# Optimization experiments

Hardware: AMD Instinct MI355X
Metric: run time of the kernel (lower is better)

Reference implementation:

```python
import jax, jax.numpy as jnp
import numpy as np

N = 25000      # nodes
E = 400000     # directed edges (avg degree 16)
FN = 32        # node feature dim
FE = 16        # edge feature dim
H = 16         # hidden_state_size
M = 16         # message_size
ITERS = 3      # mp_iterations


def setup_inputs() -> dict:
    key = jax.random.key(0)
    ks = jax.random.split(key, 16)
    s = 0.1
    return {
        "node_features": jax.random.normal(ks[0], (N, FN), jnp.float32),
        "edge_features": jax.random.normal(ks[1], (E, FE), jnp.float32),
        # Initial dense
        "W_init": jax.random.normal(ks[2], (FN, H), jnp.float32) * s,
        "b_init": jnp.zeros((H,), jnp.float32),
        # edge_net dense: FE -> M*H
        "W_edge": jax.random.normal(ks[3], (FE, M * H), jnp.float32) * s,
        "b_edge": jnp.zeros((M * H,), jnp.float32),
        # GRU (keras default, reset_after=True), input dim 1, units H, gate order z|r|h
        "Wi_gru": jax.random.normal(ks[4], (1, 3 * H), jnp.float32) * s,
        "Wh_gru": jax.random.normal(ks[5], (H, 3 * H), jnp.float32) * s,
        "bi_gru": jnp.zeros((3 * H,), jnp.float32),
        "bh_gru": jnp.zeros((3 * H,), jnp.float32),
        # Readout denses -> 1 output
        "W_ri": jax.random.normal(ks[6], (2 * H, 1), jnp.float32) * s,
        "b_ri": jnp.zeros((1,), jnp.float32),
        "W_rj": jax.random.normal(ks[7], (H, 1), jnp.float32) * s,
        "b_rj": jnp.zeros((1,), jnp.float32),
        # graph structure (directed edges): message to `receivers[e]` from `senders[e]`
        "receivers": jax.random.randint(ks[8], (E,), 0, N, jnp.int32),
        "senders": jax.random.randint(ks[9], (E,), 0, N, jnp.int32),
    }


def _gru_seq(seq, Wi, Wh, bi, bh):
    # seq: [N, T] sequence of scalars per node; keras GRU, reset_after=True, units=H
    n = seq.shape[0]
    xs = seq.T[:, :, None]  # [T, N, 1]
    h0 = jnp.zeros((n, H), seq.dtype)

    def step(h, x_t):
        gx = x_t @ Wi + bi            # [N, 3H]
        gh = h @ Wh + bh              # [N, 3H]
        xz, xr, xh = jnp.split(gx, 3, axis=1)
        hz, hr, hh = jnp.split(gh, 3, axis=1)
        z = jax.nn.sigmoid(xz + hz)
        r = jax.nn.sigmoid(xr + hr)
        hcand = jnp.tanh(xh + r * hh)
        h_new = z * h + (1.0 - z) * hcand
        return h_new, None

    h_final, _ = jax.lax.scan(step, h0, xs)
    return h_final


def reference(node_features, edge_features, W_init, b_init, W_edge, b_edge,
              Wi_gru, Wh_gru, bi_gru, bh_gru, W_ri, b_ri, W_rj, b_rj,
              receivers, senders):
    # Initial hidden state
    hidden0 = node_features @ W_init + b_init   # [N, H]
    hidden = hidden0

    # edge_net(edge) reshaped to per-edge matrices [E, M, H] (constant across iterations)
    edge_mats = (edge_features @ W_edge + b_edge).reshape(E, M, H)

    for _ in range(ITERS):
        h_nb = hidden[senders]                                  # [E, H]
        msg = jnp.einsum("emh,eh->em", edge_mats, h_nb)        # [E, M] matvec per edge
        messages = jax.ops.segment_sum(msg, receivers, num_segments=N)  # sum aggregation
        seq = jnp.concatenate([hidden, messages], axis=1)       # [N, H+M]
        hidden = _gru_seq(seq, Wi_gru, Wh_gru, bi_gru, bh_gru)  # [N, H]

    # Readout
    i = jnp.concatenate([hidden, hidden0], axis=1) @ W_ri + b_ri  # [N, 1]
    j = hidden @ W_rj + b_rj                                      # [N, 1]
    return jnp.sum(i * j, axis=0)                                 # [1]
```

## Files before the change

kernel.cpp:

```cpp
#include <hip/hip_runtime.h>

#define N_NODES 25000
#define N_EDGES 400000

__device__ __forceinline__ float fast_sigmoid(float x) {
    return __builtin_amdgcn_rcpf(1.0f + __expf(-x));
}
__device__ __forceinline__ float fast_tanh(float x) {
    return 1.0f - 2.0f * __builtin_amdgcn_rcpf(__expf(2.0f * x) + 1.0f);
}

#define SWZF(x, k) __int_as_float(__builtin_amdgcn_ds_swizzle(__float_as_int(x), ((k) << 10) | 0x1F))
#define BCAST16(x, t) __int_as_float(__builtin_amdgcn_ds_swizzle(__float_as_int(x), ((t) << 5) | 0x10))

__global__ void __launch_bounds__(256) k_init(
        const float* __restrict__ nf, const float* __restrict__ Wini,
        const float* __restrict__ bini,
        float* __restrict__ hidden0, float* __restrict__ hid,
        int* __restrict__ cnt, int* __restrict__ rcnt)
{
    int gtid = blockIdx.x * 256 + threadIdx.x;
    if (gtid <= N_NODES) { cnt[gtid] = 0; rcnt[gtid] = 0; }
    int node = gtid >> 4;
    int j = gtid & 15;
    if (node >= N_NODES) return;

    const float4* nf4 = (const float4*)(nf + node * 32);
    float acc = bini[j];
#pragma unroll
    for (int g = 0; g < 8; ++g) {
        float4 v = nf4[g];
        acc = fmaf(v.x, Wini[(g*4+0)*16 + j], acc);
        acc = fmaf(v.y, Wini[(g*4+1)*16 + j], acc);
        acc = fmaf(v.z, Wini[(g*4+2)*16 + j], acc);
        acc = fmaf(v.w, Wini[(g*4+3)*16 + j], acc);
    }
    hidden0[node*16 + j] = acc;
    hid[node*16 + j] = acc;
}

__global__ void __launch_bounds__(256) k_rank(const int* __restrict__ send,
        const int* __restrict__ recv,
        int* __restrict__ cnt, int* __restrict__ rcnt,
        int* __restrict__ rank_s, int* __restrict__ rank_r)
{
    int e = blockIdx.x * 256 + threadIdx.x;
    if (e < N_EDGES) {
        rank_s[e] = atomicAdd(&cnt[send[e]], 1);
        rank_r[e] = atomicAdd(&rcnt[recv[e]], 1);
    }
}

#define SCAN_TOT 25600
__global__ void __launch_bounds__(1024) k_scan2(
        const int* __restrict__ cnt,  int* __restrict__ row_ptr,
        const int* __restrict__ rcnt, int* __restrict__ rrow_ptr,
        float* __restrict__ out)
{
    __shared__ int data[SCAN_TOT];
    __shared__ int sums[1024];
    int t = threadIdx.x;
    const int CH = 25;

    const int* SRC = blockIdx.x ? rcnt : cnt;
    int* DST = blockIdx.x ? rrow_ptr : row_ptr;

    for (int i = t; i < SCAN_TOT; i += 1024)
        data[i] = (i < N_NODES) ? SRC[i] : 0;
    __syncthreads();

    int base = t * CH;
    int s = 0;
#pragma unroll
    for (int i = 0; i < CH; ++i) s += data[base + i];
    sums[t] = s;
    __syncthreads();

    for (int off = 1; off < 1024; off <<= 1) {
        int add = (t >= off) ? sums[t - off] : 0;
        __syncthreads();
        sums[t] += add;
        __syncthreads();
    }
    int run = sums[t] - s;

#pragma unroll
    for (int i = 0; i < CH; ++i) {
        int v = data[base + i];
        data[base + i] = run;
        run += v;
    }
    __syncthreads();

    for (int i = t; i < N_NODES; i += 1024)
        DST[i] = data[i];
    if (t == 0) {
        if (blockIdx.x == 0) { row_ptr[N_NODES] = N_EDGES; out[0] = 0.0f; }
        else                 { rrow_ptr[N_NODES] = N_EDGES; }
    }
}

__global__ void __launch_bounds__(256) k_place(const int* __restrict__ send,
        const int* __restrict__ recv,
        const int* __restrict__ rank_s, const int* __restrict__ rank_r,
        const int* __restrict__ row_ptr, const int* __restrict__ rrow_ptr,
        int* __restrict__ ipos, int* __restrict__ rp)
{
    int e = blockIdx.x * 256 + threadIdx.x;
    if (e < N_EDGES) {
        int pos = row_ptr[send[e]] + rank_s[e];
        ipos[e] = pos;
        rp[pos] = rrow_ptr[recv[e]] + rank_r[e];
    }
}

__global__ void __launch_bounds__(256) k_permute(const float* __restrict__ ef,
        const int* __restrict__ ipos, float* __restrict__ efp)
{
    int gtid = blockIdx.x * 256 + threadIdx.x;
    int e = gtid >> 4;
    int c = gtid & 15;
    if (e < N_EDGES) efp[(size_t)ipos[e]*16 + c] = ef[(size_t)e*16 + c];
}

#define MCHUNK 512
#define MSG16(E0,E1,E2,E3) ( \
    ( fmaf((E0).w,q[3],  fmaf((E0).z,q[2],  fmaf((E0).y,q[1],  fmaf((E0).x,q[0],  qb)))) \
    + fmaf((E1).w,q[7],  fmaf((E1).z,q[6],  fmaf((E1).y,q[5],  fmaf((E1).x,q[4],  0.0f)))) ) \
  + ( fmaf((E2).w,q[11], fmaf((E2).z,q[10], fmaf((E2).y,q[9],  fmaf((E2).x,q[8],  0.0f)))) \
    + fmaf((E3).w,q[15], fmaf((E3).z,q[14], fmaf((E3).y,q[13], fmaf((E3).x,q[12], 0.0f)))) ) )

__global__ void __launch_bounds__(256) k_msg(
        const float* __restrict__ hid, const float* __restrict__ efp,
        const int* __restrict__ rp,
        const float* __restrict__ We, const float* __restrict__ be,
        const int* __restrict__ row_ptr,
        float* __restrict__ tmp)
{
    __shared__ float sef[MCHUNK * 16];
    __shared__ int   srp[MCHUNK];
    int tid = threadIdx.x;
    int grp = tid >> 4;
    int m   = tid & 15;
    int s   = blockIdx.x * 16 + grp;
    bool active = (s < N_NODES);
    int sc = active ? s : 0;

    int s0 = blockIdx.x * 16;
    int blk_beg = row_ptr[s0];
    int s1 = s0 + 16; if (s1 > N_NODES) s1 = N_NODES;
    int blk_end = row_ptr[s1];

    int beg = active ? row_ptr[s]     : 0;
    int end = active ? row_ptr[s + 1] : 0;

    float h[16];
    {
        const float4* h4 = (const float4*)(hid + sc*16);
        float4 a = h4[0], b = h4[1], c = h4[2], d = h4[3];
        h[0]=a.x; h[1]=a.y; h[2]=a.z;  h[3]=a.w;
        h[4]=b.x; h[5]=b.y; h[6]=b.z;  h[7]=b.w;
        h[8]=c.x; h[9]=c.y; h[10]=c.z; h[11]=c.w;
        h[12]=d.x; h[13]=d.y; h[14]=d.z; h[15]=d.w;
    }
    float q[16];
#pragma unroll
    for (int f = 0; f < 16; ++f) {
        const float4* wf = (const float4*)(We + f*256 + m*16);
        float4 a = wf[0], b = wf[1], c = wf[2], d = wf[3];
        float acc;
        acc  = a.x*h[0]  + a.y*h[1]  + a.z*h[2]  + a.w*h[3];
        acc += b.x*h[4]  + b.y*h[5]  + b.z*h[6]  + b.w*h[7];
        acc += c.x*h[8]  + c.y*h[9]  + c.z*h[10] + c.w*h[11];
        acc += d.x*h[12] + d.y*h[13] + d.z*h[14] + d.w*h[15];
        q[f] = acc;
    }
    float qb;
    {
        const float4* bf = (const float4*)(be + m*16);
        float4 a = bf[0], b = bf[1], c = bf[2], d = bf[3];
        qb  = a.x*h[0]  + a.y*h[1]  + a.z*h[2]  + a.w*h[3];
        qb += b.x*h[4]  + b.y*h[5]  + b.z*h[6]  + b.w*h[7];
        qb += c.x*h[8]  + c.y*h[9]  + c.z*h[10] + c.w*h[11];
        qb += d.x*h[12] + d.y*h[13] + d.z*h[14] + d.w*h[15];
    }

    for (int cbeg = blk_beg; cbeg < blk_end; cbeg += MCHUNK) {
        int cend = cbeg + MCHUNK; if (cend > blk_end) cend = blk_end;
        int nedge = cend - cbeg;
        int nfl = nedge * 4;
        __syncthreads();
        {
            const float4* gsrc = (const float4*)(efp + (size_t)cbeg * 16);
            float4* ldst = (float4*)sef;
            for (int i = tid; i < nfl; i += 256) ldst[i] = gsrc[i];
            for (int i = tid; i < nedge; i += 256) srp[i] = rp[cbeg + i];
        }
        __syncthreads();

        int lo = beg > cbeg ? beg : cbeg;
        int hi = end < cend ? end : cend;
        int i = lo;
        for (; i + 2 <= hi; i += 2) {
            const float4* l0 = (const float4*)(sef + (size_t)(i   - cbeg) * 16);
            const float4* l1 = (const float4*)(sef + (size_t)(i+1 - cbeg) * 16);
            float4 A0=l0[0], A1=l0[1], A2=l0[2], A3=l0[3];
            float4 B0=l1[0], B1=l1[1], B2=l1[2], B3=l1[3];
            int r0 = srp[i   - cbeg];
            int r1 = srp[i+1 - cbeg];
            float v0 = MSG16(A0, A1, A2, A3);
            float v1 = MSG16(B0, B1, B2, B3);
            tmp[(size_t)r0*16 + m] = v0;
            tmp[(size_t)r1*16 + m] = v1;
        }
        for (; i < hi; ++i) {
            const float4* l0 = (const float4*)(sef + (size_t)(i - cbeg) * 16);
            float4 A0=l0[0], A1=l0[1], A2=l0[2], A3=l0[3];
            int r0 = srp[i - cbeg];
            tmp[(size_t)r0*16 + m] = MSG16(A0, A1, A2, A3);
        }
    }
}

__global__ void __launch_bounds__(256) k_gru(
        const float* __restrict__ hid_in, const float* __restrict__ tmp,
        const int* __restrict__ rrow_ptr,
        const float* __restrict__ Wi, const float* __restrict__ Wh,
        const float* __restrict__ bi, const float* __restrict__ bh,
        float* __restrict__ hid_out)
{
    int gtid = blockIdx.x * 256 + threadIdx.x;
    int node = gtid >> 4;
    int j = gtid & 15;
    if (node >= N_NODES) return;

    float s0 = 0.0f, s1 = 0.0f, s2 = 0.0f, s3 = 0.0f;
    {
        int beg = rrow_ptr[node];
        int end = rrow_ptr[node + 1];
        const float* p = tmp + (size_t)beg * 16 + j;
        int d = end - beg;
        int i = 0;
        for (; i + 8 <= d; i += 8) {
            float a0 = p[(i+0)*16];
            float a1 = p[(i+1)*16];
            float a2 = p[(i+2)*16];
            float a3 = p[(i+3)*16];
            float a4 = p[(i+4)*16];
            float a5 = p[(i+5)*16];
            float a6 = p[(i+6)*16];
            float a7 = p[(i+7)*16];
            s0 += a0; s1 += a1; s2 += a2; s3 += a3;
            s0 += a4; s1 += a5; s2 += a6; s3 += a7;
        }
        for (; i < d; ++i) s0 += p[i*16];
    }
    float msg_own = (s0 + s1) + (s2 + s3);
    float h_own = hid_in[node*16 + j];

    float Wz[16], Wr[16], Wc[16];
#pragma unroll
    for (int k = 0; k < 16; ++k) {
        int l = j ^ k;
        Wz[k] = Wh[l*48 + j];
        Wr[k] = Wh[l*48 + 16 + j];
        Wc[k] = Wh[l*48 + 32 + j];
    }
    float Wiz = Wi[j], Wir = Wi[16+j], Wih = Wi[32+j];
    float cz   = bi[j] + bh[j];
    float cr   = bi[16+j] + bh[16+j];
    float bih_ = bi[32+j];
    float bhh_ = bh[32+j];

    float hn = 0.0f;

#define STEPK(k) { float v = SWZF(hn, k); \
        az = fmaf(v, Wz[k], az); ar = fmaf(v, Wr[k], ar); ac = fmaf(v, Wc[k], ac); }

#define GRUSTEP(XV) { \
        float xv = (XV); \
        float az = fmaf(xv, Wiz, cz); \
        float ar = fmaf(xv, Wir, cr); \
        float ac = bhh_; \
        az = fmaf(hn, Wz[0], az); \
        ar = fmaf(hn, Wr[0], ar); \
        ac = fmaf(hn, Wc[0], ac); \
        STEPK(1)  STEPK(2)  STEPK(3)  STEPK(4)  STEPK(5) \
        STEPK(6)  STEPK(7)  STEPK(8)  STEPK(9)  STEPK(10) \
        STEPK(11) STEPK(12) STEPK(13) STEPK(14) STEPK(15) \
        float z  = fast_sigmoid(az); \
        float r  = fast_sigmoid(ar); \
        float hc = fast_tanh(fmaf(xv, Wih, bih_) + r * ac); \
        hn = fmaf(z, hn - hc, hc); }

    GRUSTEP(BCAST16(h_own, 0))  GRUSTEP(BCAST16(h_own, 1))
    GRUSTEP(BCAST16(h_own, 2))  GRUSTEP(BCAST16(h_own, 3))
    GRUSTEP(BCAST16(h_own, 4))  GRUSTEP(BCAST16(h_own, 5))
    GRUSTEP(BCAST16(h_own, 6))  GRUSTEP(BCAST16(h_own, 7))
    GRUSTEP(BCAST16(h_own, 8))  GRUSTEP(BCAST16(h_own, 9))
    GRUSTEP(BCAST16(h_own, 10)) GRUSTEP(BCAST16(h_own, 11))
    GRUSTEP(BCAST16(h_own, 12)) GRUSTEP(BCAST16(h_own, 13))
    GRUSTEP(BCAST16(h_own, 14)) GRUSTEP(BCAST16(h_own, 15))
    GRUSTEP(BCAST16(msg_own, 0))  GRUSTEP(BCAST16(msg_own, 1))
    GRUSTEP(BCAST16(msg_own, 2))  GRUSTEP(BCAST16(msg_own, 3))
    GRUSTEP(BCAST16(msg_own, 4))  GRUSTEP(BCAST16(msg_own, 5))
    GRUSTEP(BCAST16(msg_own, 6))  GRUSTEP(BCAST16(msg_own, 7))
    GRUSTEP(BCAST16(msg_own, 8))  GRUSTEP(BCAST16(msg_own, 9))
    GRUSTEP(BCAST16(msg_own, 10)) GRUSTEP(BCAST16(msg_own, 11))
    GRUSTEP(BCAST16(msg_own, 12)) GRUSTEP(BCAST16(msg_own, 13))
    GRUSTEP(BCAST16(msg_own, 14)) GRUSTEP(BCAST16(msg_own, 15))
#undef GRUSTEP
#undef STEPK

    hid_out[node*16 + j] = hn;
}

__global__ void __launch_bounds__(256) k_readout(
        const float* __restrict__ hid, const float* __restrict__ hid0,
        const float* __restrict__ Wri, const float* __restrict__ bri,
        const float* __restrict__ Wrj, const float* __restrict__ brj,
        float* __restrict__ out)
{
    int n = blockIdx.x * 256 + threadIdx.x;
    float val = 0.0f;
    if (n < N_NODES) {
        const float4* h4 = (const float4*)(hid + n * 16);
        const float4* g4 = (const float4*)(hid0 + n * 16);
        float iv = bri[0];
        float jv = brj[0];
#pragma unroll
        for (int g = 0; g < 4; ++g) {
            float4 h  = h4[g];
            float4 h0 = g4[g];
            iv = fmaf(h.x,  Wri[g*4+0], iv);  iv = fmaf(h.y,  Wri[g*4+1], iv);
            iv = fmaf(h.z,  Wri[g*4+2], iv);  iv = fmaf(h.w,  Wri[g*4+3], iv);
            iv = fmaf(h0.x, Wri[16+g*4+0], iv); iv = fmaf(h0.y, Wri[16+g*4+1], iv);
            iv = fmaf(h0.z, Wri[16+g*4+2], iv); iv = fmaf(h0.w, Wri[16+g*4+3], iv);
            jv = fmaf(h.x,  Wrj[g*4+0], jv);  jv = fmaf(h.y,  Wrj[g*4+1], jv);
            jv = fmaf(h.z,  Wrj[g*4+2], jv);  jv = fmaf(h.w,  Wrj[g*4+3], jv);
        }
        val = iv * jv;
    }
#pragma unroll
    for (int off = 32; off > 0; off >>= 1)
        val += __shfl_xor(val, off, 64);
    __shared__ float wsum[4];
    int w = threadIdx.x >> 6;
    if ((threadIdx.x & 63) == 0) wsum[w] = val;
    __syncthreads();
    if (threadIdx.x == 0)
        atomicAdd(out, wsum[0] + wsum[1] + wsum[2] + wsum[3]);
}

extern "C" void kernel_launch(void* const* d_in, const int* in_sizes, int n_in,
                              void* d_out, int out_size, void* d_ws, size_t ws_size,
                              hipStream_t stream)
{
    const float* node_features = (const float*)d_in[0];
    const float* edge_features = (const float*)d_in[1];
    const float* W_init = (const float*)d_in[2];
    const float* b_init = (const float*)d_in[3];
    const float* W_edge = (const float*)d_in[4];
    const float* b_edge = (const float*)d_in[5];
    const float* Wi_gru = (const float*)d_in[6];
    const float* Wh_gru = (const float*)d_in[7];
    const float* bi_gru = (const float*)d_in[8];
    const float* bh_gru = (const float*)d_in[9];
    const float* W_ri = (const float*)d_in[10];
    const float* b_ri = (const float*)d_in[11];
    const float* W_rj = (const float*)d_in[12];
    const float* b_rj = (const float*)d_in[13];
    const int* receivers = (const int*)d_in[14];
    const int* senders   = (const int*)d_in[15];
    float* out = (float*)d_out;

    float* fb      = (float*)d_ws;
    float* hidden0 = fb;
    float* hidA    = fb + 400000;
    float* hidB    = fb + 800000;
    float* tmp     = fb + 1200000;
    float* efp     = fb + 7600000;
    int* ib       = (int*)(fb + 14000000);
    int* cnt      = ib;
    int* row_ptr  = ib + 25024;
    int* rcnt     = ib + 50048;
    int* rrow_ptr = ib + 75072;
    int* ipos     = ib + 100096;
    int* rp       = ib + 500096;
    int* rank_s   = ib + 900096;
    int* rank_r   = ib + 1300096;

    dim3 b256(256);
    int grid_n16 = (N_NODES * 16 + 255) / 256;
    int grid_e   = (N_EDGES + 255) / 256;
    int grid_e16 = (N_EDGES * 16 + 255) / 256;
    int grid_n   = (N_NODES + 255) / 256;
    int grid_blk = (N_NODES + 15) / 16;

    k_init<<<grid_n16, b256, 0, stream>>>(node_features, W_init, b_init,
                                          hidden0, hidA, cnt, rcnt);
    k_rank<<<grid_e, b256, 0, stream>>>(senders, receivers, cnt, rcnt,
                                        rank_s, rank_r);
    k_scan2<<<2, 1024, 0, stream>>>(cnt, row_ptr, rcnt, rrow_ptr, out);
    k_place<<<grid_e, b256, 0, stream>>>(senders, receivers, rank_s, rank_r,
                                         row_ptr, rrow_ptr, ipos, rp);
    k_permute<<<grid_e16, b256, 0, stream>>>(edge_features, ipos, efp);

    float* hin = hidA;
    float* hout = hidB;
    for (int it = 0; it < 3; ++it) {
        k_msg<<<grid_blk, b256, 0, stream>>>(hin, efp, rp,
                                             W_edge, b_edge, row_ptr, tmp);
        k_gru<<<grid_n16, b256, 0, stream>>>(hin, tmp, rrow_ptr,
                                             Wi_gru, Wh_gru, bi_gru, bh_gru, hout);
        float* t = hin; hin = hout; hout = t;
    }

    k_readout<<<grid_n, b256, 0, stream>>>(hin, hidden0, W_ri, b_ri, W_rj, b_rj, out);
}
```

Baseline: 405.3 us.

## Process two nodes per GRU thread and fuse edge permute into placement

```diff
diff --git a/kernel.cpp b/kernel.cpp
--- a/kernel.cpp
+++ b/kernel.cpp
@@ -2,6 +2,7 @@
 
 #define N_NODES 25000
 #define N_EDGES 400000
+#define NHALF   12500
 
 __device__ __forceinline__ float fast_sigmoid(float x) {
     return __builtin_amdgcn_rcpf(1.0f + __expf(-x));
@@ -11,7 +12,7 @@
 }
 
 #define SWZF(x, k) __int_as_float(__builtin_amdgcn_ds_swizzle(__float_as_int(x), ((k) << 10) | 0x1F))
-#define BCAST16(x, t) __int_as_float(__builtin_amdgcn_ds_swizzle(__float_as_int(x), ((t) << 5) | 0x10))
+#define BPERM(x, a) __int_as_float(__builtin_amdgcn_ds_bpermute((a), __float_as_int(x)))
 
 __global__ void __launch_bounds__(256) k_init(
         const float* __restrict__ nf, const float* __restrict__ Wini,
@@ -104,23 +105,18 @@
         const int* __restrict__ recv,
         const int* __restrict__ rank_s, const int* __restrict__ rank_r,
         const int* __restrict__ row_ptr, const int* __restrict__ rrow_ptr,
-        int* __restrict__ ipos, int* __restrict__ rp)
+        const float* __restrict__ ef, float* __restrict__ efp,
+        int* __restrict__ rp)
 {
     int e = blockIdx.x * 256 + threadIdx.x;
     if (e < N_EDGES) {
         int pos = row_ptr[send[e]] + rank_s[e];
-        ipos[e] = pos;
         rp[pos] = rrow_ptr[recv[e]] + rank_r[e];
-    }
-}
-
-__global__ void __launch_bounds__(256) k_permute(const float* __restrict__ ef,
-        const int* __restrict__ ipos, float* __restrict__ efp)
-{
-    int gtid = blockIdx.x * 256 + threadIdx.x;
-    int e = gtid >> 4;
-    int c = gtid & 15;
-    if (e < N_EDGES) efp[(size_t)ipos[e]*16 + c] = ef[(size_t)e*16 + c];
+        const float4* src = (const float4*)(ef + (size_t)e * 16);
+        float4* dst = (float4*)(efp + (size_t)pos * 16);
+        float4 a = src[0], b = src[1], c = src[2], d = src[3];
+        dst[0] = a; dst[1] = b; dst[2] = c; dst[3] = d;
+    }
 }
 
 #define MCHUNK 512
@@ -222,6 +218,31 @@
     }
 }
 
+__device__ __forceinline__ float gather16(const float* __restrict__ tmp,
+        const int* __restrict__ rrow_ptr, int node, int j)
+{
+    int beg = rrow_ptr[node];
+    int end = rrow_ptr[node + 1];
+    const float* p = tmp + (size_t)beg * 16 + j;
+    int d = end - beg;
+    float s0 = 0.0f, s1 = 0.0f, s2 = 0.0f, s3 = 0.0f;
+    int i = 0;
+    for (; i + 8 <= d; i += 8) {
+        float a0 = p[(i+0)*16];
+        float a1 = p[(i+1)*16];
+        float a2 = p[(i+2)*16];
+        float a3 = p[(i+3)*16];
+        float a4 = p[(i+4)*16];
+        float a5 = p[(i+5)*16];
+        float a6 = p[(i+6)*16];
+        float a7 = p[(i+7)*16];
+        s0 += a0; s1 += a1; s2 += a2; s3 += a3;
+        s0 += a4; s1 += a5; s2 += a6; s3 += a7;
+    }
+    for (; i < d; ++i) s0 += p[i*16];
+    return (s0 + s1) + (s2 + s3);
+}
+
 __global__ void __launch_bounds__(256) k_gru(
         const float* __restrict__ hid_in, const float* __restrict__ tmp,
         const int* __restrict__ rrow_ptr,
@@ -230,33 +251,15 @@
         float* __restrict__ hid_out)
 {
     int gtid = blockIdx.x * 256 + threadIdx.x;
-    int node = gtid >> 4;
+    int nA = gtid >> 4;
     int j = gtid & 15;
-    if (node >= N_NODES) return;
-
-    float s0 = 0.0f, s1 = 0.0f, s2 = 0.0f, s3 = 0.0f;
-    {
-        int beg = rrow_ptr[node];
-        int end = rrow_ptr[node + 1];
-        const float* p = tmp + (size_t)beg * 16 + j;
-        int d = end - beg;
-        int i = 0;
-        for (; i + 8 <= d; i += 8) {
-            float a0 = p[(i+0)*16];
-            float a1 = p[(i+1)*16];
-            float a2 = p[(i+2)*16];
-            float a3 = p[(i+3)*16];
-            float a4 = p[(i+4)*16];
-            float a5 = p[(i+5)*16];
-            float a6 = p[(i+6)*16];
-            float a7 = p[(i+7)*16];
-            s0 += a0; s1 += a1; s2 += a2; s3 += a3;
-            s0 += a4; s1 += a5; s2 += a6; s3 += a7;
-        }
-        for (; i < d; ++i) s0 += p[i*16];
-    }
-    float msg_own = (s0 + s1) + (s2 + s3);
-    float h_own = hid_in[node*16 + j];
+    if (nA >= NHALF) return;
+    int nB = nA + NHALF;
+
+    float msgA = gather16(tmp, rrow_ptr, nA, j);
+    float msgB = gather16(tmp, rrow_ptr, nB, j);
+    float hA = hid_in[nA*16 + j];
+    float hB = hid_in[nB*16 + j];
 
     float Wz[16], Wr[16], Wc[16];
 #pragma unroll
@@ -272,47 +275,51 @@
     float bih_ = bi[32+j];
     float bhh_ = bh[32+j];
 
-    float hn = 0.0f;
-
-#define STEPK(k) { float v = SWZF(hn, k); \
-        az = fmaf(v, Wz[k], az); ar = fmaf(v, Wr[k], ar); ac = fmaf(v, Wc[k], ac); }
-
-#define GRUSTEP(XV) { \
-        float xv = (XV); \
-        float az = fmaf(xv, Wiz, cz); \
-        float ar = fmaf(xv, Wir, cr); \
-        float ac = bhh_; \
-        az = fmaf(hn, Wz[0], az); \
-        ar = fmaf(hn, Wr[0], ar); \
-        ac = fmaf(hn, Wc[0], ac); \
-        STEPK(1)  STEPK(2)  STEPK(3)  STEPK(4)  STEPK(5) \
-        STEPK(6)  STEPK(7)  STEPK(8)  STEPK(9)  STEPK(10) \
-        STEPK(11) STEPK(12) STEPK(13) STEPK(14) STEPK(15) \
-        float z  = fast_sigmoid(az); \
-        float r  = fast_sigmoid(ar); \
-        float hc = fast_tanh(fmaf(xv, Wih, bih_) + r * ac); \
-        hn = fmaf(z, hn - hc, hc); }
-
-    GRUSTEP(BCAST16(h_own, 0))  GRUSTEP(BCAST16(h_own, 1))
-    GRUSTEP(BCAST16(h_own, 2))  GRUSTEP(BCAST16(h_own, 3))
-    GRUSTEP(BCAST16(h_own, 4))  GRUSTEP(BCAST16(h_own, 5))
-    GRUSTEP(BCAST16(h_own, 6))  GRUSTEP(BCAST16(h_own, 7))
-    GRUSTEP(BCAST16(h_own, 8))  GRUSTEP(BCAST16(h_own, 9))
-    GRUSTEP(BCAST16(h_own, 10)) GRUSTEP(BCAST16(h_own, 11))
-    GRUSTEP(BCAST16(h_own, 12)) GRUSTEP(BCAST16(h_own, 13))
-    GRUSTEP(BCAST16(h_own, 14)) GRUSTEP(BCAST16(h_own, 15))
-    GRUSTEP(BCAST16(msg_own, 0))  GRUSTEP(BCAST16(msg_own, 1))
-    GRUSTEP(BCAST16(msg_own, 2))  GRUSTEP(BCAST16(msg_own, 3))
-    GRUSTEP(BCAST16(msg_own, 4))  GRUSTEP(BCAST16(msg_own, 5))
-    GRUSTEP(BCAST16(msg_own, 6))  GRUSTEP(BCAST16(msg_own, 7))
-    GRUSTEP(BCAST16(msg_own, 8))  GRUSTEP(BCAST16(msg_own, 9))
-    GRUSTEP(BCAST16(msg_own, 10)) GRUSTEP(BCAST16(msg_own, 11))
-    GRUSTEP(BCAST16(msg_own, 12)) GRUSTEP(BCAST16(msg_own, 13))
-    GRUSTEP(BCAST16(msg_own, 14)) GRUSTEP(BCAST16(msg_own, 15))
-#undef GRUSTEP
-#undef STEPK
-
-    hid_out[node*16 + j] = hn;
+    float hnA = 0.0f, hnB = 0.0f;
+    int baddr = ((threadIdx.x & 63) & 0x30) << 2;
+
+#define STEPK2(k) { \
+        float vA = SWZF(hnA, k); float vB = SWZF(hnB, k); \
+        azA = fmaf(vA, Wz[k], azA); azB = fmaf(vB, Wz[k], azB); \
+        arA = fmaf(vA, Wr[k], arA); arB = fmaf(vB, Wr[k], arB); \
+        acA = fmaf(vA, Wc[k], acA); acB = fmaf(vB, Wc[k], acB); }
+
+#define GRUSTEP2(XA, XB) { \
+        float azA = fmaf((XA), Wiz, cz),  azB = fmaf((XB), Wiz, cz); \
+        float arA = fmaf((XA), Wir, cr),  arB = fmaf((XB), Wir, cr); \
+        float acA = bhh_, acB = bhh_; \
+        azA = fmaf(hnA, Wz[0], azA); azB = fmaf(hnB, Wz[0], azB); \
+        arA = fmaf(hnA, Wr[0], arA); arB = fmaf(hnB, Wr[0], arB); \
+        acA = fmaf(hnA, Wc[0], acA); acB = fmaf(hnB, Wc[0], acB); \
+        STEPK2(1)  STEPK2(2)  STEPK2(3)  STEPK2(4)  STEPK2(5) \
+        STEPK2(6)  STEPK2(7)  STEPK2(8)  STEPK2(9)  STEPK2(10) \
+        STEPK2(11) STEPK2(12) STEPK2(13) STEPK2(14) STEPK2(15) \
+        float zA = fast_sigmoid(azA), zB = fast_sigmoid(azB); \
+        float rA = fast_sigmoid(arA), rB = fast_sigmoid(arB); \
+        float hcA = fast_tanh(fmaf((XA), Wih, bih_) + rA * acA); \
+        float hcB = fast_tanh(fmaf((XB), Wih, bih_) + rB * acB); \
+        hnA = fmaf(zA, hnA - hcA, hcA); \
+        hnB = fmaf(zB, hnB - hcB, hcB); }
+
+#pragma unroll 1
+    for (int t = 0; t < 16; ++t) {
+        int a = baddr + (t << 2);
+        float xA = BPERM(hA, a);
+        float xB = BPERM(hB, a);
+        GRUSTEP2(xA, xB)
+    }
+#pragma unroll 1
+    for (int t = 0; t < 16; ++t) {
+        int a = baddr + (t << 2);
+        float xA = BPERM(msgA, a);
+        float xB = BPERM(msgB, a);
+        GRUSTEP2(xA, xB)
+    }
+#undef GRUSTEP2
+#undef STEPK2
+
+    hid_out[nA*16 + j] = hnA;
+    hid_out[nB*16 + j] = hnB;
 }
 
 __global__ void __launch_bounds__(256) k_readout(
@@ -385,17 +392,16 @@
     int* row_ptr  = ib + 25024;
     int* rcnt     = ib + 50048;
     int* rrow_ptr = ib + 75072;
-    int* ipos     = ib + 100096;
-    int* rp       = ib + 500096;
-    int* rank_s   = ib + 900096;
-    int* rank_r   = ib + 1300096;
+    int* rp       = ib + 100096;
+    int* rank_s   = ib + 500096;
+    int* rank_r   = ib + 900096;
 
     dim3 b256(256);
     int grid_n16 = (N_NODES * 16 + 255) / 256;
     int grid_e   = (N_EDGES + 255) / 256;
-    int grid_e16 = (N_EDGES * 16 + 255) / 256;
     int grid_n   = (N_NODES + 255) / 256;
     int grid_blk = (N_NODES + 15) / 16;
+    int grid_gru = (NHALF * 16 + 255) / 256;
 
     k_init<<<grid_n16, b256, 0, stream>>>(node_features, W_init, b_init,
                                           hidden0, hidA, cnt, rcnt);
@@ -403,15 +409,15 @@
                                         rank_s, rank_r);
     k_scan2<<<2, 1024, 0, stream>>>(cnt, row_ptr, rcnt, rrow_ptr, out);
     k_place<<<grid_e, b256, 0, stream>>>(senders, receivers, rank_s, rank_r,
-                                         row_ptr, rrow_ptr, ipos, rp);
-    k_permute<<<grid_e16, b256, 0, stream>>>(edge_features, ipos, efp);
+                                         row_ptr, rrow_ptr,
+                                         edge_features, efp, rp);
 
     float* hin = hidA;
     float* hout = hidB;
     for (int it = 0; it < 3; ++it) {
         k_msg<<<grid_blk, b256, 0, stream>>>(hin, efp, rp,
                                              W_edge, b_edge, row_ptr, tmp);
-        k_gru<<<grid_n16, b256, 0, stream>>>(hin, tmp, rrow_ptr,
+        k_gru<<<grid_gru, b256, 0, stream>>>(hin, tmp, rrow_ptr,
                                              Wi_gru, Wh_gru, bi_gru, bh_gru, hout);
         float* t = hin; hin = hout; hout = t;
     }
```

After: 433.2 us. +6.9%, slower.
